# Kernel optimization log

Hardware: AMD Instinct MI355X
Metric: run time of the kernel (lower is better)

Reference implementation:

```python
import jax, jax.numpy as jnp
import numpy as np

HIDDEN = 512
HEADS = 8


def setup_inputs() -> dict:
    key = jax.random.key(0)
    ks = jax.random.split(key, 7)
    B, S, D = 4, 2048, HIDDEN
    scale = 1.0 / np.sqrt(D)
    return {
        "src": jax.random.normal(ks[0], (B, S, D), dtype=jnp.float32),
        "Wq": jax.random.normal(ks[1], (D, D), dtype=jnp.float32) * scale,
        "bq": jax.random.normal(ks[2], (D,), dtype=jnp.float32) * 0.01,
        "Wk": jax.random.normal(ks[3], (D, D), dtype=jnp.float32) * scale,
        "bk": jax.random.normal(ks[4], (D,), dtype=jnp.float32) * 0.01,
        "Wv": jax.random.normal(ks[5], (D, D), dtype=jnp.float32) * scale,
        "bv": jax.random.normal(ks[6], (D,), dtype=jnp.float32) * 0.01,
    }


def reference(src, Wq, bq, Wk, bk, Wv, bv):
    B, S, D = src.shape
    H = HEADS
    hd = D // H
    # QKV projections -> [B, S, H, hd]
    q = (src @ Wq + bq).reshape(B, S, H, hd)
    k = (src @ Wk + bk).reshape(B, S, H, hd)
    v = (src @ Wv + bv).reshape(B, S, H, hd)
    # scores [B, H, S, S]; note: NO causal mask (matches original module)
    scores = jnp.einsum("bqhd,bkhd->bhqk", q, k) / jnp.sqrt(jnp.asarray(hd, src.dtype))
    attn = jax.nn.softmax(scores, axis=-1)
    out = jnp.einsum("bhqk,bkhd->bqhd", attn, v)
    return out.reshape(B, S, D)
```

## Files before the change

### kernel.cpp

```cpp
#include <hip/hip_runtime.h>

typedef __bf16 bf16;
typedef __bf16 bf16x8 __attribute__((ext_vector_type(8)));
typedef __bf16 bf16x4 __attribute__((ext_vector_type(4)));
typedef float f32x4 __attribute__((ext_vector_type(4)));
typedef float f32x16 __attribute__((ext_vector_type(16)));
typedef unsigned int u32;

#define QK_SCALE 0.1803368801111204f

__device__ __forceinline__ int rc16(int row, int g) {
    return row * 256 + ((g ^ (row & 15)) << 4);
}
__device__ __forceinline__ int swzb(int row, int col) {
    return (((row) << 7) + ((col) << 1)) ^ (((row) & 7) << 4);
}

__device__ __forceinline__ void gload_lds16(const void* g, void* l) {
    __builtin_amdgcn_global_load_lds(
        (const __attribute__((address_space(1))) unsigned int*)g,
        (__attribute__((address_space(3))) unsigned int*)l, 16, 0, 0);
}

__device__ __forceinline__ u32 cvtpk(float lo, float hi) {
    u32 r;
    asm("v_cvt_pk_bf16_f32 %0, %1, %2" : "=v"(r) : "v"(lo), "v"(hi));
    return r;
}
__device__ __forceinline__ void pl32swap(u32& a, u32& b) {
    asm("v_permlane32_swap_b32 %0, %1" : "+v"(a), "+v"(b));
}

__global__ __launch_bounds__(256) void cast_src(const float* __restrict__ x,
                                                bf16* __restrict__ y) {
    int i = blockIdx.x * 256 + threadIdx.x;
    float4 v = reinterpret_cast<const float4*>(x)[i];
    bf16x4 p;
    p[0] = (bf16)v.x; p[1] = (bf16)v.y; p[2] = (bf16)v.z; p[3] = (bf16)v.w;
    reinterpret_cast<bf16x4*>(y)[i] = p;
}

__global__ __launch_bounds__(256) void wtrans_all(const float* __restrict__ Wq,
                                                  const float* __restrict__ Wk,
                                                  const float* __restrict__ Wv,
                                                  bf16* __restrict__ Wt_all) {
    __shared__ float T[64][65];
    const int w = blockIdx.z;
    const float* W = w == 0 ? Wq : (w == 1 ? Wk : Wv);
    const float wsc = (w == 0) ? QK_SCALE : 1.0f;
    bf16* Wt = Wt_all + (size_t)w * 512 * 512;
    const int k0 = blockIdx.x * 64, n0 = blockIdx.y * 64;
    const int tx = threadIdx.x & 63, ty = threadIdx.x >> 6;
#pragma unroll
    for (int i = 0; i < 16; ++i) {
        int row = ty * 16 + i;
        T[row][tx] = W[(size_t)(k0 + row) * 512 + n0 + tx];
    }
    __syncthreads();
#pragma unroll
    for (int i = 0; i < 16; ++i) {
        int row = ty * 16 + i;
        Wt[(size_t)(n0 + row) * 512 + k0 + tx] = (bf16)(T[tx][row] * wsc);
    }
}

__global__ __launch_bounds__(256) void qkv_gemm_all(const bf16* __restrict__ srcb,
                                                    const bf16* __restrict__ Wt_all,
                                                    const float* __restrict__ bq,
                                                    const float* __restrict__ bk,
                                                    const float* __restrict__ bv,
                                                    bf16* __restrict__ Qb,
                                                    bf16* __restrict__ Kb,
                                                    bf16* __restrict__ Vtb) {
    __shared__ __align__(16) bf16 As[128 * 64];
    __shared__ __align__(16) bf16 Bs[128 * 64];
    const int t = threadIdx.x, lane = t & 63, wid = t >> 6;
    const int m0 = blockIdx.x * 128;
    const int n0g = blockIdx.y * 128;
    const int oi = n0g >> 9, n0 = n0g & 511;
    const float* bias = oi == 0 ? bq : (oi == 1 ? bk : bv);
    const float bsc = (oi == 0) ? QK_SCALE : 1.0f;
    bf16* outp = oi == 0 ? Qb : (oi == 1 ? Kb : Vtb);
    const bf16* Wt = Wt_all + (size_t)oi * 512 * 512;
    const bool sw = (oi == 2);
    const int wm = (wid >> 1) * 64, wn = (wid & 1) * 64;
    const int fr = lane & 15, fq = lane >> 4;

    f32x4 acc[4][4] = {};

    for (int k0 = 0; k0 < 512; k0 += 64) {
        __syncthreads();
#pragma unroll
        for (int c = 0; c < 4; ++c) {
            int u = (wid * 4 + c) * 64 + lane;
            int row = u >> 3;
            int slot = (u & 7) ^ (row & 7);
            gload_lds16(srcb + (size_t)(m0 + row) * 512 + k0 + slot * 8,
                        (char*)As + (wid * 4 + c) * 1024);
            gload_lds16(Wt + (size_t)(n0 + row) * 512 + k0 + slot * 8,
                        (char*)Bs + (wid * 4 + c) * 1024);
        }
        __syncthreads();

        bf16x8 a[2][4], b[2][4];
#pragma unroll
        for (int c = 0; c < 2; ++c)
#pragma unroll
            for (int i = 0; i < 4; ++i) {
                a[c][i] = *reinterpret_cast<const bf16x8*>(
                    (const char*)As + swzb(wm + i * 16 + fr, c * 32 + fq * 8));
                b[c][i] = *reinterpret_cast<const bf16x8*>(
                    (const char*)Bs + swzb(wn + i * 16 + fr, c * 32 + fq * 8));
            }
        if (!sw) {
#pragma unroll
            for (int i = 0; i < 4; ++i)
#pragma unroll
                for (int j = 0; j < 4; ++j)
#pragma unroll
                    for (int c = 0; c < 2; ++c)
                        acc[i][j] = __builtin_amdgcn_mfma_f32_16x16x32_bf16(a[c][i], b[c][j], acc[i][j], 0, 0, 0);
        } else {
#pragma unroll
            for (int i = 0; i < 4; ++i)
#pragma unroll
                for (int j = 0; j < 4; ++j)
#pragma unroll
                    for (int c = 0; c < 2; ++c)
                        acc[i][j] = __builtin_amdgcn_mfma_f32_16x16x32_bf16(b[c][j], a[c][i], acc[i][j], 0, 0, 0);
        }
    }

    if (!sw) {
#pragma unroll
        for (int j = 0; j < 4; ++j) {
            int n = n0 + wn + j * 16 + fr;
            float bj = bias[n] * bsc;
            int h = n >> 6, d = n & 63;
#pragma unroll
            for (int i = 0; i < 4; ++i)
#pragma unroll
                for (int r = 0; r < 4; ++r) {
                    int m = m0 + wm + i * 16 + fq * 4 + r;
                    int b_ = m >> 11, s = m & 2047;
                    outp[(((size_t)(b_ * 8 + h)) * 2048 + s) * 64 + d] =
                        (bf16)(acc[i][j][r] + bj);
                }
        }
    } else {
#pragma unroll
        for (int j = 0; j < 4; ++j)
#pragma unroll
            for (int r = 0; r < 4; ++r) {
                int n = n0 + wn + j * 16 + fq * 4 + r;
                float bj = bias[n];
                int h = n >> 6, d = n & 63;
#pragma unroll
                for (int i = 0; i < 4; ++i) {
                    int m = m0 + wm + i * 16 + fr;
                    int b_ = m >> 11, s = m & 2047;
                    outp[(((size_t)(b_ * 8 + h)) * 64 + d) * 2048 + s] =
                        (bf16)(acc[i][j][r] + bj);
                }
            }
    }
}

__global__ __launch_bounds__(512, 2) void attn_fwd(const bf16* __restrict__ Q,
                                                   const bf16* __restrict__ K,
                                                   const bf16* __restrict__ Vt,
                                                   float* __restrict__ out) {
    __shared__ __align__(16) char lds_raw[65536 + 1024];
    const int t = threadIdx.x, lane = t & 63, wid = t >> 6;
    const int grp = wid >> 2, w4 = wid & 3;
    const int c31 = lane & 31, h = lane >> 5;
    const int bh = blockIdx.x & 31;
    const int qchunk = blockIdx.x >> 5;
    const int qw = qchunk * 256 + w4 * 64;

    bf16x8 qf0[4], qf1[4];
    {
        const bf16* Qp0 = Q + ((size_t)bh * 2048 + qw + c31) * 64;
        const bf16* Qp1 = Qp0 + 32 * 64;
#pragma unroll
        for (int ks = 0; ks < 4; ++ks) {
            qf0[ks] = *reinterpret_cast<const bf16x8*>(&Qp0[ks * 16 + h * 8]);
            qf1[ks] = *reinterpret_cast<const bf16x8*>(&Qp1[ks * 16 + h * 8]);
        }
    }

    bf16x8 bones;
#pragma unroll
    for (int e = 0; e < 8; ++e) bones[e] = (bf16)1.0f;

    f32x16 acc_o[2][2] = {};
    f32x16 acc_l[2] = {};

    const char* Kpb0 = (const char*)(K + (size_t)bh * 2048 * 64);
    const char* Vpb0 = (const char*)(Vt + (size_t)bh * 64 * 2048);

    auto stage = [&](int buf, int tt) {
        const size_t kv0 = (size_t)(grp * 1024 + tt * 64);
        const char* Kg = Kpb0 + kv0 * 128;
        const char* Vg = Vpb0 + kv0 * 2;
        char* Kl = lds_raw + (grp * 2 + buf) * 8192;
        char* Vl = lds_raw + 32768 + (grp * 2 + buf) * 8192;
#pragma unroll
        for (int c = 0; c < 2; ++c) {
            int ch = w4 * 2 + c;
            int r = ch * 4 + (lane >> 4);
            int g = (lane & 15) ^ (r & 15);
            gload_lds16(Kg + r * 256 + g * 16, Kl + ch * 1024);
            gload_lds16(Vg + (size_t)(2 * r + (g >> 3)) * 4096 + (g & 7) * 16,
                        Vl + ch * 1024);
        }
    };

    const int rq = c31 >> 1, gb = (c31 & 1) * 8;

    auto compute = [&](int buf) {
        const char* Kl = lds_raw + (grp * 2 + buf) * 8192;
        const char* Vl = lds_raw + 32768 + (grp * 2 + buf) * 8192;

        f32x16 s00 = {}, s01 = {}, s10 = {}, s11 = {};
        __builtin_amdgcn_s_setprio(1);
#pragma unroll
        for (int ks = 0; ks < 4; ++ks) {
            int g = gb + ks * 2 + h;
            bf16x8 kf0 = *reinterpret_cast<const bf16x8*>(Kl + rc16(rq, g));
            s00 = __builtin_amdgcn_mfma_f32_32x32x16_bf16(kf0, qf0[ks], s00, 0, 0, 0);
            s10 = __builtin_amdgcn_mfma_f32_32x32x16_bf16(kf0, qf1[ks], s10, 0, 0, 0);
            bf16x8 kf1 = *reinterpret_cast<const bf16x8*>(Kl + rc16(16 + rq, g));
            s01 = __builtin_amdgcn_mfma_f32_32x32x16_bf16(kf1, qf0[ks], s01, 0, 0, 0);
            s11 = __builtin_amdgcn_mfma_f32_32x32x16_bf16(kf1, qf1[ks], s11, 0, 0, 0);
        }
        __builtin_amdgcn_s_setprio(0);

        bf16x8 pa0[4], pa1[4];
#pragma unroll
        for (int st = 0; st < 2; ++st) {
            f32x16& sa = st ? s10 : s00;
            f32x16& sb = st ? s11 : s01;
#pragma unroll
            for (int r = 0; r < 16; ++r) {
                sa[r] = __builtin_amdgcn_exp2f(sa[r]);
                sb[r] = __builtin_amdgcn_exp2f(sb[r]);
            }
#pragma unroll
            for (int ktl = 0; ktl < 2; ++ktl) {
                const f32x16& sv = ktl ? sb : sa;
#pragma unroll
                for (int k2 = 0; k2 < 2; ++k2) {
                    u32 X = cvtpk(sv[8 * k2 + 0], sv[8 * k2 + 1]);
                    u32 Y = cvtpk(sv[8 * k2 + 4], sv[8 * k2 + 5]);
                    u32 Z = cvtpk(sv[8 * k2 + 2], sv[8 * k2 + 3]);
                    u32 W = cvtpk(sv[8 * k2 + 6], sv[8 * k2 + 7]);
                    pl32swap(X, Y);
                    pl32swap(Z, W);
                    union { bf16x8 v; u32 w[4]; } pu;
                    pu.w[0] = X; pu.w[1] = Z; pu.w[2] = Y; pu.w[3] = W;
                    if (st) pa1[ktl * 2 + k2] = pu.v;
                    else    pa0[ktl * 2 + k2] = pu.v;
                }
            }
        }

        __builtin_amdgcn_s_setprio(1);
#pragma unroll
        for (int kg = 0; kg < 4; ++kg) {
            int g = gb + kg * 2 + h;
            bf16x8 vf0 = *reinterpret_cast<const bf16x8*>(Vl + rc16(rq, g));
            acc_o[0][0] = __builtin_amdgcn_mfma_f32_32x32x16_bf16(pa0[kg], vf0, acc_o[0][0], 0, 0, 0);
            acc_o[1][0] = __builtin_amdgcn_mfma_f32_32x32x16_bf16(pa1[kg], vf0, acc_o[1][0], 0, 0, 0);
            bf16x8 vf1 = *reinterpret_cast<const bf16x8*>(Vl + rc16(16 + rq, g));
            acc_o[0][1] = __builtin_amdgcn_mfma_f32_32x32x16_bf16(pa0[kg], vf1, acc_o[0][1], 0, 0, 0);
            acc_o[1][1] = __builtin_amdgcn_mfma_f32_32x32x16_bf16(pa1[kg], vf1, acc_o[1][1], 0, 0, 0);
            acc_l[0] = __builtin_amdgcn_mfma_f32_32x32x16_bf16(pa0[kg], bones, acc_l[0], 0, 0, 0);
            acc_l[1] = __builtin_amdgcn_mfma_f32_32x32x16_bf16(pa1[kg], bones, acc_l[1], 0, 0, 0);
        }
        __builtin_amdgcn_s_setprio(0);
    };

    stage(0, 0);
    __syncthreads();

    for (int tt = 0; tt < 16; tt += 2) {
        stage(1, tt + 1);
        compute(0);
        __syncthreads();
        if (tt + 2 < 16) stage(0, tt + 2);
        compute(1);
        __syncthreads();
    }

    float* Os = (float*)lds_raw;
    float* Ls = (float*)(lds_raw + 65536);
    if (grp == 1) {
#pragma unroll
        for (int st = 0; st < 2; ++st)
#pragma unroll
            for (int reg = 0; reg < 16; ++reg) {
                int qr = (reg & 3) + 8 * (reg >> 2) + 4 * h;
                int ql = w4 * 64 + st * 32 + qr;
                Os[ql * 64 + c31]      = acc_o[st][0][reg];
                Os[ql * 64 + 32 + c31] = acc_o[st][1][reg];
                if (c31 == 0) Ls[ql] = acc_l[st][reg];
            }
    }
    __syncthreads();
    if (grp == 0) {
        const int b_ = bh >> 3, hh = bh & 7;
#pragma unroll
        for (int st = 0; st < 2; ++st)
#pragma unroll
            for (int reg = 0; reg < 16; ++reg) {
                int qr = (reg & 3) + 8 * (reg >> 2) + 4 * h;
                int ql = w4 * 64 + st * 32 + qr;
                float l = acc_l[st][reg] + Ls[ql];
                float inv = __builtin_amdgcn_rcpf(l);
                int s_ = qchunk * 256 + ql;
                size_t base = ((size_t)b_ * 2048 + s_) * 512 + hh * 64;
                out[base + c31] =
                    (acc_o[st][0][reg] + Os[ql * 64 + c31]) * inv;
                out[base + 32 + c31] =
                    (acc_o[st][1][reg] + Os[ql * 64 + 32 + c31]) * inv;
            }
    }
}

extern "C" void kernel_launch(void* const* d_in, const int* in_sizes, int n_in,
                              void* d_out, int out_size, void* d_ws, size_t ws_size,
                              hipStream_t stream) {
    const float* src = (const float*)d_in[0];
    const float* Wq  = (const float*)d_in[1];
    const float* bq  = (const float*)d_in[2];
    const float* Wk  = (const float*)d_in[3];
    const float* bk  = (const float*)d_in[4];
    const float* Wv  = (const float*)d_in[5];
    const float* bv  = (const float*)d_in[6];
    float* out = (float*)d_out;

    char* ws = (char*)d_ws;
    const size_t WT_SZ  = 512u * 512u * sizeof(bf16);
    const size_t QKV_SZ = 8192u * 512u * sizeof(bf16);
    bf16* WtA  = (bf16*)(ws);
    bf16* srcb = (bf16*)(ws + 3 * WT_SZ);
    bf16* Qb   = (bf16*)(ws + 3 * WT_SZ + QKV_SZ);
    bf16* Kb   = (bf16*)(ws + 3 * WT_SZ + 2 * QKV_SZ);
    bf16* Vtb  = (bf16*)(ws + 3 * WT_SZ + 3 * QKV_SZ);

    cast_src<<<4096, 256, 0, stream>>>(src, srcb);
    wtrans_all<<<dim3(8, 8, 3), 256, 0, stream>>>(Wq, Wk, Wv, WtA);

    qkv_gemm_all<<<dim3(64, 12), 256, 0, stream>>>(srcb, WtA, bq, bk, bv, Qb, Kb, Vtb);

    attn_fwd<<<256, 512, 0, stream>>>(Qb, Kb, Vtb, out);
}
```

Measured before the change: 76.85 us.

## Stage QKV GEMM epilogue through LDS and compute softmax row sums with VALU

The QKV projection epilogue now writes accumulators into a swizzled LDS tile, then issues coalesced 16-byte global stores for Q/K and the transposed V layout, replacing scattered 2-byte stores. In the attention kernel, the row-sum of exponentiated scores is accumulated with VALU adds plus a permlane32 swap instead of two extra MFMAs against a ones vector per kv group. This removes a quarter of the PV-phase MFMA work and makes the GEMM writes wide. The cost is extra VALU work, an added LDS round trip and barrier in the GEMM, and row sums taken in fp32 before bf16 rounding, which differs slightly from the old bf16-product sums.

```diff
diff --git a/kernel.cpp b/kernel.cpp
--- a/kernel.cpp
+++ b/kernel.cpp
@@ -14,6 +14,9 @@
 }
 __device__ __forceinline__ int swzb(int row, int col) {
     return (((row) << 7) + ((col) << 1)) ^ (((row) & 7) << 4);
+}
+__device__ __forceinline__ int csw(int row, int colbyte) {
+    return row * 256 + (colbyte ^ ((row & 7) << 4));
 }
 
 __device__ __forceinline__ void gload_lds16(const void* g, void* l) {
@@ -72,8 +75,9 @@
                                                     bf16* __restrict__ Qb,
                                                     bf16* __restrict__ Kb,
                                                     bf16* __restrict__ Vtb) {
-    __shared__ __align__(16) bf16 As[128 * 64];
-    __shared__ __align__(16) bf16 Bs[128 * 64];
+    __shared__ __align__(16) char gl[32768];
+    bf16* As = (bf16*)gl;
+    bf16* Bs = (bf16*)(gl + 16384);
     const int t = threadIdx.x, lane = t & 63, wid = t >> 6;
     const int m0 = blockIdx.x * 128;
     const int n0g = blockIdx.y * 128;
@@ -131,19 +135,19 @@
         }
     }
 
+    __syncthreads();
+    char* Cs = gl;
     if (!sw) {
 #pragma unroll
         for (int j = 0; j < 4; ++j) {
-            int n = n0 + wn + j * 16 + fr;
-            float bj = bias[n] * bsc;
-            int h = n >> 6, d = n & 63;
+            float bj = bias[n0 + wn + j * 16 + fr] * bsc;
 #pragma unroll
             for (int i = 0; i < 4; ++i)
 #pragma unroll
                 for (int r = 0; r < 4; ++r) {
-                    int m = m0 + wm + i * 16 + fq * 4 + r;
-                    int b_ = m >> 11, s = m & 2047;
-                    outp[(((size_t)(b_ * 8 + h)) * 2048 + s) * 64 + d] =
+                    int row = wm + i * 16 + fq * 4 + r;
+                    int colb = (wn + j * 16 + fr) * 2;
+                    *reinterpret_cast<bf16*>(Cs + csw(row, colb)) =
                         (bf16)(acc[i][j][r] + bj);
                 }
         }
@@ -152,17 +156,33 @@
         for (int j = 0; j < 4; ++j)
 #pragma unroll
             for (int r = 0; r < 4; ++r) {
-                int n = n0 + wn + j * 16 + fq * 4 + r;
-                float bj = bias[n];
-                int h = n >> 6, d = n & 63;
+                float bj = bias[n0 + wn + j * 16 + fq * 4 + r];
 #pragma unroll
                 for (int i = 0; i < 4; ++i) {
-                    int m = m0 + wm + i * 16 + fr;
-                    int b_ = m >> 11, s = m & 2047;
-                    outp[(((size_t)(b_ * 8 + h)) * 64 + d) * 2048 + s] =
+                    int row = wn + j * 16 + fq * 4 + r;
+                    int colb = (wm + i * 16 + fr) * 2;
+                    *reinterpret_cast<bf16*>(Cs + csw(row, colb)) =
                         (bf16)(acc[i][j][r] + bj);
                 }
             }
+    }
+    __syncthreads();
+
+    const int b_ = m0 >> 11, sbase = m0 & 2047, h0 = n0 >> 6;
+#pragma unroll
+    for (int it = 0; it < 8; ++it) {
+        int u = it * 256 + t;
+        int row = u >> 4, c = u & 15;
+        bf16x8 val = *reinterpret_cast<const bf16x8*>(Cs + csw(row, c * 16));
+        size_t addr;
+        if (!sw) {
+            addr = ((size_t)((b_ * 8 + h0 + (c >> 3)) * 2048 + sbase + row)) * 64
+                   + (c & 7) * 8;
+        } else {
+            addr = ((size_t)((b_ * 8 + h0 + (row >> 6)) * 64 + (row & 63))) * 2048
+                   + sbase + c * 8;
+        }
+        *reinterpret_cast<bf16x8*>(outp + addr) = val;
     }
 }
 
@@ -170,7 +190,7 @@
                                                    const bf16* __restrict__ K,
                                                    const bf16* __restrict__ Vt,
                                                    float* __restrict__ out) {
-    __shared__ __align__(16) char lds_raw[65536 + 1024];
+    __shared__ __align__(16) char lds_raw[65536 + 2048];
     const int t = threadIdx.x, lane = t & 63, wid = t >> 6;
     const int grp = wid >> 2, w4 = wid & 3;
     const int c31 = lane & 31, h = lane >> 5;
@@ -189,12 +209,8 @@
         }
     }
 
-    bf16x8 bones;
-#pragma unroll
-    for (int e = 0; e < 8; ++e) bones[e] = (bf16)1.0f;
-
     f32x16 acc_o[2][2] = {};
-    f32x16 acc_l[2] = {};
+    float l_run[2] = {0.f, 0.f};
 
     const char* Kpb0 = (const char*)(K + (size_t)bh * 2048 * 64);
     const char* Vpb0 = (const char*)(Vt + (size_t)bh * 64 * 2048);
@@ -246,6 +262,20 @@
                 sa[r] = __builtin_amdgcn_exp2f(sa[r]);
                 sb[r] = __builtin_amdgcn_exp2f(sb[r]);
             }
+            float p0 = 0.f, p1 = 0.f, p2 = 0.f, p3 = 0.f;
+#pragma unroll
+            for (int r = 0; r < 16; r += 4) {
+                p0 += sa[r]; p1 += sa[r + 1]; p2 += sa[r + 2]; p3 += sa[r + 3];
+            }
+#pragma unroll
+            for (int r = 0; r < 16; r += 4) {
+                p0 += sb[r]; p1 += sb[r + 1]; p2 += sb[r + 2]; p3 += sb[r + 3];
+            }
+            float ps = (p0 + p1) + (p2 + p3);
+            u32 ua = __builtin_bit_cast(u32, ps), ub = ua;
+            pl32swap(ua, ub);
+            l_run[st] += __builtin_bit_cast(float, ua) + __builtin_bit_cast(float, ub);
+
 #pragma unroll
             for (int ktl = 0; ktl < 2; ++ktl) {
                 const f32x16& sv = ktl ? sb : sa;
@@ -275,8 +305,6 @@
             bf16x8 vf1 = *reinterpret_cast<const bf16x8*>(Vl + rc16(16 + rq, g));
             acc_o[0][1] = __builtin_amdgcn_mfma_f32_32x32x16_bf16(pa0[kg], vf1, acc_o[0][1], 0, 0, 0);
             acc_o[1][1] = __builtin_amdgcn_mfma_f32_32x32x16_bf16(pa1[kg], vf1, acc_o[1][1], 0, 0, 0);
-            acc_l[0] = __builtin_amdgcn_mfma_f32_32x32x16_bf16(pa0[kg], bones, acc_l[0], 0, 0, 0);
-            acc_l[1] = __builtin_amdgcn_mfma_f32_32x32x16_bf16(pa1[kg], bones, acc_l[1], 0, 0, 0);
         }
         __builtin_amdgcn_s_setprio(0);
     };
@@ -293,8 +321,16 @@
         __syncthreads();
     }
 
-    float* Os = (float*)lds_raw;
-    float* Ls = (float*)(lds_raw + 65536);
+    float* Os  = (float*)lds_raw;
+    float* Ls0 = (float*)(lds_raw + 65536);
+    float* Ls1 = (float*)(lds_raw + 66560);
+    {
+        float* Lsg = grp ? Ls1 : Ls0;
+        if (h == 0) {
+            Lsg[w4 * 64 + c31]      = l_run[0];
+            Lsg[w4 * 64 + 32 + c31] = l_run[1];
+        }
+    }
     if (grp == 1) {
 #pragma unroll
         for (int st = 0; st < 2; ++st)
@@ -304,7 +340,6 @@
                 int ql = w4 * 64 + st * 32 + qr;
                 Os[ql * 64 + c31]      = acc_o[st][0][reg];
                 Os[ql * 64 + 32 + c31] = acc_o[st][1][reg];
-                if (c31 == 0) Ls[ql] = acc_l[st][reg];
             }
     }
     __syncthreads();
@@ -316,7 +351,7 @@
             for (int reg = 0; reg < 16; ++reg) {
                 int qr = (reg & 3) + 8 * (reg >> 2) + 4 * h;
                 int ql = w4 * 64 + st * 32 + qr;
-                float l = acc_l[st][reg] + Ls[ql];
+                float l = Ls0[ql] + Ls1[ql];
                 float inv = __builtin_amdgcn_rcpf(l);
                 int s_ = qchunk * 256 + ql;
                 size_t base = ((size_t)b_ * 2048 + s_) * 512 + hh * 64;
```

Result: no change. 77.50 us (+0.8%).
